# Optimization experiments

Measured on AMD Instinct MI355X. Metric: run time of the kernel, lower is better.

## Reference

```python
import jax, jax.numpy as jnp
import numpy as np

TEMPERATURE = 0.07
NUM_HARD_NEGATIVES = 5
BATCH, DIM = 4096, 768


def setup_inputs() -> dict:
    key = jax.random.key(0)
    k1, k2 = jax.random.split(key)
    return {
        "text_emb": jax.random.normal(k1, (BATCH, DIM), dtype=jnp.float32),
        "table_emb": jax.random.normal(k2, (BATCH, DIM), dtype=jnp.float32),
    }


def _ttcl_loss(text_emb, table_emb):
    # F.normalize(dim=1)
    t = text_emb / jnp.linalg.norm(text_emb, axis=1, keepdims=True)
    z = table_emb / jnp.linalg.norm(table_emb, axis=1, keepdims=True)
    sim = z @ t.T  # [B, B], sim[i, j] = <table_i, text_j>
    B = sim.shape[0]
    pos = jnp.diagonal(sim) / TEMPERATURE  # [B], <text_i, table_i> == <table_i, text_i>
    diag_mask = jnp.eye(B, dtype=bool)
    neg_inf = jnp.finfo(sim.dtype).min

    def hard_neg_loss(neg_rows):
        # neg_rows[i] holds the B candidate negatives for sample i; exclude self.
        neg = jnp.where(diag_mask, neg_inf, neg_rows)
        top_vals, _ = jax.lax.top_k(neg, NUM_HARD_NEGATIVES)  # [B, k]
        logits = jnp.concatenate([pos[:, None], top_vals / TEMPERATURE], axis=1)  # [B, k+1]
        # cross_entropy with label 0 == -log_softmax(logits)[:, 0]
        return -jax.nn.log_softmax(logits, axis=1)[:, 0]

    # t2z: negatives for i are sim[j][i], j != i  -> column i -> rows of sim.T
    loss_t2z = jnp.sum(hard_neg_loss(sim.T))
    # z2t: negatives for i are sim[i][j], j != i  -> row i
    loss_z2t = jnp.sum(hard_neg_loss(sim))
    loss = (loss_t2z + loss_z2t) / (2 * B)
    return loss, sim


def reference(text_emb, table_emb):
    return _ttcl_loss(text_emb, table_emb)
```

## Files before the change

kernel.cpp:

```cpp
#include <hip/hip_runtime.h>
#include <stdint.h>
#include <math.h>

#define BSZ 4096
#define DIM 768
#define TEMP 0.07f

typedef short short8 __attribute__((ext_vector_type(8)));
typedef short short4v __attribute__((ext_vector_type(4)));
typedef float f32x4 __attribute__((ext_vector_type(4)));


__device__ __forceinline__ uint16_t f2bf(float f) {
  uint32_t u = __float_as_uint(f);
  uint32_t r = (u + 0x7FFFu + ((u >> 16) & 1u)) >> 16;
  return (uint16_t)r;
}

__device__ __forceinline__ void gll16(const void* g, void* l) {
  __builtin_amdgcn_global_load_lds(
      (__attribute__((address_space(1))) void*)(uintptr_t)g,
      (__attribute__((address_space(3))) void*)l,
      16, 0, 0);
}

__device__ __forceinline__ void ins5(float v, float& a, float& b, float& c,
                                     float& d, float& e) {
  if (v > e) {
    e = v;
    if (e > d) { float t = d; d = e; e = t;
      if (d > c) { t = c; c = d; d = t;
        if (c > b) { t = b; b = c; c = t;
          if (b > a) { t = a; a = b; b = t; } } } }
  }
}

__device__ __forceinline__ void sins5(float v, float& a, float& b, float& c,
                                      float& d, float& e) {
  float t;
  t = fmaxf(a, v); v = fminf(a, v); a = t;
  t = fmaxf(b, v); v = fminf(b, v); b = t;
  t = fmaxf(c, v); v = fminf(c, v); c = t;
  t = fmaxf(d, v); v = fminf(d, v); d = t;
  e = fmaxf(e, v);
}

__global__ __launch_bounds__(192) void k_norm(const float* __restrict__ text,
                                              const float* __restrict__ table,
                                              uint16_t* __restrict__ tn,
                                              uint16_t* __restrict__ zn) {
  int row = blockIdx.x & (BSZ - 1);
  bool isTable = blockIdx.x >= BSZ;
  const float* src = (isTable ? table : text) + (size_t)row * DIM;
  uint16_t* dst = (isTable ? zn : tn) + (size_t)row * DIM;
  int tid = threadIdx.x;

  f32x4 v = *(const f32x4*)(src + tid * 4);
  float ss = v[0] * v[0] + v[1] * v[1] + v[2] * v[2] + v[3] * v[3];
  #pragma unroll
  for (int off = 32; off >= 1; off >>= 1) ss += __shfl_xor(ss, off);
  __shared__ float wss[3];
  if ((tid & 63) == 0) wss[tid >> 6] = ss;
  __syncthreads();
  float inv = rsqrtf(wss[0] + wss[1] + wss[2]);
  short4v o;
  o[0] = (short)f2bf(v[0] * inv);
  o[1] = (short)f2bf(v[1] * inv);
  o[2] = (short)f2bf(v[2] * inv);
  o[3] = (short)f2bf(v[3] * inv);
  *(short4v*)(dst + tid * 4) = o;
}

__global__ __launch_bounds__(512, 2) void k_gemm(const uint16_t* __restrict__ Zb,
                                                 const uint16_t* __restrict__ Tb,
                                                 float* __restrict__ sim) {
  extern __shared__ __attribute__((aligned(16))) char lds[];

  int tid = threadIdx.x;
  int wave = tid >> 6, lane = tid & 63;
  int wm = wave >> 2, wn = wave & 3;

  int bid = blockIdx.x;
  int xcd = bid & 7, li = bid >> 3;
  int brow = (((xcd >> 1) << 2) + (li >> 3)) << 8;
  int bcol = (((xcd & 1) << 3) + (li & 7)) << 8;

  f32x4 acc[8][4] = {};

  const uint16_t* gA = Zb + (size_t)brow * DIM;
  const uint16_t* gB = Tb + (size_t)bcol * DIM;

  int r7 = lane & 7;
  int kqg = lane >> 4;
  int rlo = lane & 15;

  int srow = (wave << 5) + (lane >> 3);
  int sc = ((lane & 7) ^ (srow & 7)) << 3;

  auto SA = [&](int t, int bb, int j) {
    gll16(gA + (size_t)(srow + j * 8) * DIM + t * 64 + sc,
          lds + bb + (wave << 12) + (j << 10));
  };
  auto SB = [&](int t, int bb, int j) {
    gll16(gB + (size_t)(srow + j * 8) * DIM + t * 64 + sc,
          lds + bb + 32768 + (wave << 12) + (j << 10));
  };

  auto LOADB = [&](int bb, short8 (&bf)[2][4]) {
    const char* Bb = lds + bb + 32768;
    #pragma unroll
    for (int ks = 0; ks < 2; ++ks) {
      int ch = (((ks << 2) + kqg) ^ r7) << 4;
      #pragma unroll
      for (int n = 0; n < 4; ++n) {
        int R = (wn << 6) + (n << 4) + rlo;
        bf[ks][n] = *(const short8*)(Bb + (R << 7) + ch);
      }
    }
  };
  auto PHASE = [&](int bb, int mlo, short8 (&bf)[2][4]) {
    __builtin_amdgcn_s_setprio(1);
    #pragma unroll
    for (int ks = 0; ks < 2; ++ks) {
      int ch = (((ks << 2) + kqg) ^ r7) << 4;
      #pragma unroll
      for (int mm = 0; mm < 4; ++mm) {
        int R = (wm << 7) + ((mlo + mm) << 4) + rlo;
        short8 af = *(const short8*)(lds + bb + (R << 7) + ch);
        #pragma unroll
        for (int n = 0; n < 4; ++n)
          acc[mlo + mm][n] = __builtin_amdgcn_mfma_f32_16x16x32_bf16(
              af, bf[ks][n], acc[mlo + mm][n], 0, 0, 0);
      }
    }
    __builtin_amdgcn_s_setprio(0);
  };

  #pragma unroll
  for (int j = 0; j < 4; ++j) { SA(0, 0, j); SB(0, 0, j); }
  #pragma unroll
  for (int j = 0; j < 4; ++j) { SA(1, 65536, j); SB(1, 65536, j); }
  asm volatile("s_waitcnt vmcnt(8)" ::: "memory");
  __builtin_amdgcn_s_barrier();

  #pragma unroll 2
  for (int t = 0; t < 10; ++t) {
    int bb = (t & 1) << 16;
    short8 bf[2][4];
    LOADB(bb, bf);
    PHASE(bb, 0, bf);
    __builtin_amdgcn_s_barrier();
    if ((wave & 2) == 0) {
      SA(t + 2, bb, 0); SA(t + 2, bb, 1); SA(t + 2, bb, 2); SA(t + 2, bb, 3);
    }
    SB(t + 2, bb, 0); SB(t + 2, bb, 1);
    SB(t + 2, bb, 2); SB(t + 2, bb, 3);
    PHASE(bb, 4, bf);
    __builtin_amdgcn_s_barrier();
    if ((wave & 2) != 0) {
      SA(t + 2, bb, 0); SA(t + 2, bb, 1); SA(t + 2, bb, 2); SA(t + 2, bb, 3);
    }
    asm volatile("s_waitcnt vmcnt(8)" ::: "memory");
    __builtin_amdgcn_s_barrier();
  }

  {
    short8 bf[2][4];
    LOADB(0, bf);
    PHASE(0, 0, bf);
    PHASE(0, 4, bf);
  }
  asm volatile("s_waitcnt vmcnt(0)" ::: "memory");
  __builtin_amdgcn_s_barrier();
  {
    short8 bf[2][4];
    LOADB(65536, bf);
    PHASE(65536, 0, bf);
    PHASE(65536, 4, bf);
  }

  int crow0 = brow + (wm << 7) + ((lane >> 4) << 2);
  int ccol0 = bcol + (wn << 6) + (lane & 15);
  #pragma unroll
  for (int m = 0; m < 8; ++m)
    #pragma unroll
    for (int n = 0; n < 4; ++n)
      #pragma unroll
      for (int r = 0; r < 4; ++r)
        sim[(size_t)(crow0 + m * 16 + r) * BSZ + (ccol0 + n * 16)] = acc[m][n][r];
}

__global__ __launch_bounds__(256) void k_tile(const float* __restrict__ sim,
                                              float* __restrict__ rp,
                                              float* __restrict__ cp) {
  extern __shared__ float l32[];
  int tid = threadIdx.x;

  int xcd = blockIdx.x & 7, li = blockIdx.x >> 3;
  int tr = ((xcd >> 1) << 4) + (li >> 4);
  int tc = ((xcd & 1) << 4) + (li & 15);
  int row0 = tr << 6, col0 = tc << 7;
  bool diag = ((tr >> 1) == tc);
  int lcbase = (tr & 1) << 6;

  int q = tid & 31;
  int g = tid >> 5;
  const float* gsrc = sim + (size_t)(row0 + (g << 3)) * BSZ + col0 + (q << 2);

  f32x4 v[8];
  #pragma unroll
  for (int k = 0; k < 8; ++k)
    v[k] = *(const f32x4*)(gsrc + (size_t)k * BSZ);

  #pragma unroll
  for (int k = 0; k < 8; ++k) {
    int r = (g << 3) + k;
    int lc = lcbase + r;
    if (diag && (lc >> 2) == q) v[k][lc & 3] = -1e30f;
    *(f32x4*)(l32 + (r << 7) + ((q ^ (r & 7)) << 2)) = v[k];
  }
  __syncthreads();

  {
    int row = tid >> 2, h = tid & 3;
    int rx = row & 7;
    const float* rb = l32 + (row << 7);
    float a0 = -1e30f, a1 = -1e30f, a2 = -1e30f, a3 = -1e30f, a4 = -1e30f;
    #pragma unroll
    for (int j = 0; j < 8; ++j) {
      int c16 = (h << 3) + j;
      f32x4 x = *(const f32x4*)(rb + ((c16 ^ rx) << 2));
      sins5(x[0], a0, a1, a2, a3, a4);
      sins5(x[1], a0, a1, a2, a3, a4);
      sins5(x[2], a0, a1, a2, a3, a4);
      sins5(x[3], a0, a1, a2, a3, a4);
    }
    #pragma unroll
    for (int xr = 1; xr <= 2; xr <<= 1) {
      float b0 = __shfl_xor(a0, xr), b1 = __shfl_xor(a1, xr),
            b2 = __shfl_xor(a2, xr), b3 = __shfl_xor(a3, xr),
            b4 = __shfl_xor(a4, xr);
      sins5(b0, a0, a1, a2, a3, a4);
      sins5(b1, a0, a1, a2, a3, a4);
      sins5(b2, a0, a1, a2, a3, a4);
      sins5(b3, a0, a1, a2, a3, a4);
      sins5(b4, a0, a1, a2, a3, a4);
    }
    if (h == 0) {
      float* pr = rp + ((size_t)(row0 + row) * 32 + tc) * 5;
      pr[0] = a0; pr[1] = a1; pr[2] = a2; pr[3] = a3; pr[4] = a4;
    }
  }

  {
    int c = tid >> 1, hf = tid & 1;
    int cc = c >> 2, cw = c & 3;
    float a0 = -1e30f, a1 = -1e30f, a2 = -1e30f, a3 = -1e30f, a4 = -1e30f;
    #pragma unroll 8
    for (int k = 0; k < 32; ++k) {
      int r = (hf << 5) + k;
      float x = l32[(r << 7) + (((cc ^ (r & 7)) << 2) | cw)];
      sins5(x, a0, a1, a2, a3, a4);
    }
    float b0 = __shfl_xor(a0, 1), b1 = __shfl_xor(a1, 1),
          b2 = __shfl_xor(a2, 1), b3 = __shfl_xor(a3, 1),
          b4 = __shfl_xor(a4, 1);
    sins5(b0, a0, a1, a2, a3, a4);
    sins5(b1, a0, a1, a2, a3, a4);
    sins5(b2, a0, a1, a2, a3, a4);
    sins5(b3, a0, a1, a2, a3, a4);
    sins5(b4, a0, a1, a2, a3, a4);
    if (hf == 0) {
      float* pc = cp + ((size_t)(col0 + c) * 64 + tr) * 5;
      pc[0] = a0; pc[1] = a1; pc[2] = a2; pc[3] = a3; pc[4] = a4;
    }
  }
}

__global__ __launch_bounds__(256) void k_merge(const float* __restrict__ sim,
                                               const float* __restrict__ rp,
                                               const float* __restrict__ cp,
                                               float* __restrict__ lossbuf) {
  int wave = threadIdx.x >> 6, lane = threadIdx.x & 63;
  int wid = blockIdx.x * 4 + wave;
  bool isCol = wid >= BSZ;
  int line = isCol ? wid - BSZ : wid;

  float t0 = -1e30f, t1 = -1e30f, t2 = -1e30f, t3 = -1e30f, t4 = -1e30f;
  if (isCol) {
    const float* src = cp + (size_t)line * 320;
    ins5(src[lane], t0, t1, t2, t3, t4);
    ins5(src[lane + 64], t0, t1, t2, t3, t4);
    ins5(src[lane + 128], t0, t1, t2, t3, t4);
    ins5(src[lane + 192], t0, t1, t2, t3, t4);
    ins5(src[lane + 256], t0, t1, t2, t3, t4);
  } else {
    const float* src = rp + (size_t)line * 160;
    ins5(src[lane], t0, t1, t2, t3, t4);
    ins5(src[lane + 64], t0, t1, t2, t3, t4);
    if (lane < 32) ins5(src[lane + 128], t0, t1, t2, t3, t4);
  }

  float top[5];
  #pragma unroll
  for (int e = 0; e < 5; e++) {
    float m = t0;
    #pragma unroll
    for (int off = 32; off >= 1; off >>= 1) m = fmaxf(m, __shfl_xor(m, off));
    unsigned long long msk = __ballot(t0 == m);
    int owner = __ffsll(msk) - 1;
    if (lane == owner) { t0 = t1; t1 = t2; t2 = t3; t3 = t4; t4 = -1e30f; }
    top[e] = m;
  }

  if (lane == 0) {
    float pos = sim[(size_t)line * BSZ + line] / TEMP;
    float l0 = top[0] / TEMP, l1 = top[1] / TEMP, l2 = top[2] / TEMP,
          l3 = top[3] / TEMP, l4 = top[4] / TEMP;
    float mx = fmaxf(pos, fmaxf(fmaxf(l0, l1), fmaxf(fmaxf(l2, l3), l4)));
    float s = expf(pos - mx) + expf(l0 - mx) + expf(l1 - mx) +
              expf(l2 - mx) + expf(l3 - mx) + expf(l4 - mx);
    lossbuf[wid] = mx + logf(s) - pos;
  }
}

__global__ __launch_bounds__(256) void k_reduce(const float* __restrict__ losses,
                                                float* __restrict__ out) {
  int tid = threadIdx.x;
  float s = 0.f;
  for (int i = tid; i < 2 * BSZ; i += 256) s += losses[i];
  #pragma unroll
  for (int off = 32; off >= 1; off >>= 1) s += __shfl_xor(s, off);
  __shared__ float wss[4];
  if ((tid & 63) == 0) wss[tid >> 6] = s;
  __syncthreads();
  if (tid == 0) out[0] = (wss[0] + wss[1] + wss[2] + wss[3]) / (2.0f * BSZ);
}

extern "C" void kernel_launch(void* const* d_in, const int* in_sizes, int n_in,
                              void* d_out, int out_size, void* d_ws, size_t ws_size,
                              hipStream_t stream) {
  const float* text = (const float*)d_in[0];
  const float* table = (const float*)d_in[1];
  float* out = (float*)d_out;
  float* sim = out + 1;

  uint16_t* Zb = (uint16_t*)d_ws;
  uint16_t* Tb = Zb + (size_t)BSZ * DIM;
  float* lossbuf = (float*)(Tb + (size_t)BSZ * DIM);

  float* rp = (float*)d_ws;
  float* cp = rp + (size_t)BSZ * 32 * 5;

  k_norm<<<2 * BSZ, 192, 0, stream>>>(text, table, Tb, Zb);
  k_gemm<<<(BSZ / 256) * (BSZ / 256), 512, 131072, stream>>>(Zb, Tb, sim);
  k_tile<<<(BSZ / 64) * (BSZ / 128), 256, 32768, stream>>>(sim, rp, cp);
  k_merge<<<2 * BSZ / 4, 256, 0, stream>>>(sim, rp, cp, lossbuf);
  k_reduce<<<1, 256, 0, stream>>>(lossbuf, out);
}
```

Measured before the change: 82.88 us.

## Single-buffer GEMM LDS staging to halve shared memory and raise occupancy

The bf16 GEMM drops its double-buffered 128KB LDS staging for a single 64KB buffer. Refills of the next K tile are split across extra barriers so B and the two halves of A are reloaded as each is consumed. The launch-bounds occupancy hint rises from 2 to 4 so more blocks can share a CU. The cost is less overlap between global loads and MFMA work, more barriers per iteration, and possible register pressure or spills from the tighter bound. The grid is only 256 blocks, so the extra occupancy may never be used.

Result: slower. 289.6 us (+249.5%).

```diff
diff --git a/kernel.cpp b/kernel.cpp
--- a/kernel.cpp
+++ b/kernel.cpp
@@ -71,7 +71,7 @@
   *(short4v*)(dst + tid * 4) = o;
 }
 
-__global__ __launch_bounds__(512, 2) void k_gemm(const uint16_t* __restrict__ Zb,
+__global__ __launch_bounds__(512, 4) void k_gemm(const uint16_t* __restrict__ Zb,
                                                  const uint16_t* __restrict__ Tb,
                                                  float* __restrict__ sim) {
   extern __shared__ __attribute__((aligned(16))) char lds[];
@@ -96,18 +96,19 @@
 
   int srow = (wave << 5) + (lane >> 3);
   int sc = ((lane & 7) ^ (srow & 7)) << 3;
-
-  auto SA = [&](int t, int bb, int j) {
+  bool ownH1 = (wave & 2) == 0;
+
+  auto SA = [&](int t, int j) {
     gll16(gA + (size_t)(srow + j * 8) * DIM + t * 64 + sc,
-          lds + bb + (wave << 12) + (j << 10));
+          lds + (wave << 12) + (j << 10));
   };
-  auto SB = [&](int t, int bb, int j) {
+  auto SB = [&](int t, int j) {
     gll16(gB + (size_t)(srow + j * 8) * DIM + t * 64 + sc,
-          lds + bb + 32768 + (wave << 12) + (j << 10));
+          lds + 32768 + (wave << 12) + (j << 10));
   };
 
-  auto LOADB = [&](int bb, short8 (&bf)[2][4]) {
-    const char* Bb = lds + bb + 32768;
+  auto LOADB = [&](short8 (&bf)[2][4]) {
+    const char* Bb = lds + 32768;
     #pragma unroll
     for (int ks = 0; ks < 2; ++ks) {
       int ch = (((ks << 2) + kqg) ^ r7) << 4;
@@ -118,7 +119,7 @@
       }
     }
   };
-  auto PHASE = [&](int bb, int mlo, short8 (&bf)[2][4]) {
+  auto PHASE = [&](int mlo, short8 (&bf)[2][4]) {
     __builtin_amdgcn_s_setprio(1);
     #pragma unroll
     for (int ks = 0; ks < 2; ++ks) {
@@ -126,7 +127,7 @@
       #pragma unroll
       for (int mm = 0; mm < 4; ++mm) {
         int R = (wm << 7) + ((mlo + mm) << 4) + rlo;
-        short8 af = *(const short8*)(lds + bb + (R << 7) + ch);
+        short8 af = *(const short8*)(lds + (R << 7) + ch);
         #pragma unroll
         for (int n = 0; n < 4; ++n)
           acc[mlo + mm][n] = __builtin_amdgcn_mfma_f32_16x16x32_bf16(
@@ -136,48 +137,43 @@
     __builtin_amdgcn_s_setprio(0);
   };
 
-  #pragma unroll
-  for (int j = 0; j < 4; ++j) { SA(0, 0, j); SB(0, 0, j); }
-  #pragma unroll
-  for (int j = 0; j < 4; ++j) { SA(1, 65536, j); SB(1, 65536, j); }
-  asm volatile("s_waitcnt vmcnt(8)" ::: "memory");
-  __builtin_amdgcn_s_barrier();
-
-  #pragma unroll 2
-  for (int t = 0; t < 10; ++t) {
-    int bb = (t & 1) << 16;
+#define BAR __builtin_amdgcn_s_barrier()
+#define VM4 asm volatile("s_waitcnt vmcnt(4)" ::: "memory")
+
+  #pragma unroll
+  for (int j = 0; j < 4; ++j) { SA(0, j); SB(0, j); }
+  asm volatile("s_waitcnt vmcnt(0)" ::: "memory");
+  BAR;
+
+  #pragma unroll 1
+  for (int t = 0; t <= 10; ++t) {
     short8 bf[2][4];
-    LOADB(bb, bf);
-    PHASE(bb, 0, bf);
-    __builtin_amdgcn_s_barrier();
-    if ((wave & 2) == 0) {
-      SA(t + 2, bb, 0); SA(t + 2, bb, 1); SA(t + 2, bb, 2); SA(t + 2, bb, 3);
-    }
-    SB(t + 2, bb, 0); SB(t + 2, bb, 1);
-    SB(t + 2, bb, 2); SB(t + 2, bb, 3);
-    PHASE(bb, 4, bf);
-    __builtin_amdgcn_s_barrier();
-    if ((wave & 2) != 0) {
-      SA(t + 2, bb, 0); SA(t + 2, bb, 1); SA(t + 2, bb, 2); SA(t + 2, bb, 3);
-    }
-    asm volatile("s_waitcnt vmcnt(8)" ::: "memory");
-    __builtin_amdgcn_s_barrier();
+    LOADB(bf);
+    BAR;
+    SB(t + 1, 0); SB(t + 1, 1); SB(t + 1, 2); SB(t + 1, 3);
+    if (ownH1) VM4;
+    BAR;
+    PHASE(0, bf);
+    BAR;
+    if (ownH1) { SA(t + 1, 0); SA(t + 1, 1); SA(t + 1, 2); SA(t + 1, 3); }
+    else VM4;
+    BAR;
+    PHASE(4, bf);
+    BAR;
+    if (!ownH1) { SA(t + 1, 0); SA(t + 1, 1); SA(t + 1, 2); SA(t + 1, 3); }
+    if (t < 10) VM4;
+    else asm volatile("s_waitcnt vmcnt(0)" ::: "memory");
+    BAR;
   }
 
   {
     short8 bf[2][4];
-    LOADB(0, bf);
-    PHASE(0, 0, bf);
-    PHASE(0, 4, bf);
-  }
-  asm volatile("s_waitcnt vmcnt(0)" ::: "memory");
-  __builtin_amdgcn_s_barrier();
-  {
-    short8 bf[2][4];
-    LOADB(65536, bf);
-    PHASE(65536, 0, bf);
-    PHASE(65536, 4, bf);
-  }
+    LOADB(bf);
+    PHASE(0, bf);
+    PHASE(4, bf);
+  }
+#undef BAR
+#undef VM4
 
   int crow0 = brow + (wm << 7) + ((lane >> 4) << 2);
   int ccol0 = bcol + (wn << 6) + (lane & 15);
@@ -353,7 +349,7 @@
   float* cp = rp + (size_t)BSZ * 32 * 5;
 
   k_norm<<<2 * BSZ, 192, 0, stream>>>(text, table, Tb, Zb);
-  k_gemm<<<(BSZ / 256) * (BSZ / 256), 512, 131072, stream>>>(Zb, Tb, sim);
+  k_gemm<<<(BSZ / 256) * (BSZ / 256), 512, 65536, stream>>>(Zb, Tb, sim);
   k_tile<<<(BSZ / 64) * (BSZ / 128), 256, 32768, stream>>>(sim, rp, cp);
   k_merge<<<2 * BSZ / 4, 256, 0, stream>>>(sim, rp, cp, lossbuf);
   k_reduce<<<1, 256, 0, stream>>>(lossbuf, out);
```

## Fuse final loss reduction into merge via atomics and simplify GEMM prefetch schedule

Applied to the files above, without the earlier changes.

The separate single-block reduce kernel is removed. Each merge block now sums its four per-line losses in shared memory and atomically adds the scaled total to the output scalar, which the norm kernel zeroes first. Separately, the GEMM main loop no longer interleaves the next-tile global-to-LDS prefetches between its two MFMA phases. All waves now issue every prefetch after one barrier, which also drops a barrier per iteration. This saves a kernel launch but adds float-atomic contention and nondeterministic summation order, and the prefetch may now overlap less with compute.

New measurement: 93.65 us. 1.13x slower.

```diff
diff --git a/kernel.cpp b/kernel.cpp
--- a/kernel.cpp
+++ b/kernel.cpp
@@ -48,7 +48,9 @@
 __global__ __launch_bounds__(192) void k_norm(const float* __restrict__ text,
                                               const float* __restrict__ table,
                                               uint16_t* __restrict__ tn,
-                                              uint16_t* __restrict__ zn) {
+                                              uint16_t* __restrict__ zn,
+                                              float* __restrict__ out) {
+  if (blockIdx.x == 0 && threadIdx.x == 0) out[0] = 0.f;
   int row = blockIdx.x & (BSZ - 1);
   bool isTable = blockIdx.x >= BSZ;
   const float* src = (isTable ? table : text) + (size_t)row * DIM;
@@ -149,17 +151,10 @@
     short8 bf[2][4];
     LOADB(bb, bf);
     PHASE(bb, 0, bf);
-    __builtin_amdgcn_s_barrier();
-    if ((wave & 2) == 0) {
-      SA(t + 2, bb, 0); SA(t + 2, bb, 1); SA(t + 2, bb, 2); SA(t + 2, bb, 3);
-    }
-    SB(t + 2, bb, 0); SB(t + 2, bb, 1);
-    SB(t + 2, bb, 2); SB(t + 2, bb, 3);
     PHASE(bb, 4, bf);
     __builtin_amdgcn_s_barrier();
-    if ((wave & 2) != 0) {
-      SA(t + 2, bb, 0); SA(t + 2, bb, 1); SA(t + 2, bb, 2); SA(t + 2, bb, 3);
-    }
+    SA(t + 2, bb, 0); SA(t + 2, bb, 1); SA(t + 2, bb, 2); SA(t + 2, bb, 3);
+    SB(t + 2, bb, 0); SB(t + 2, bb, 1); SB(t + 2, bb, 2); SB(t + 2, bb, 3);
     asm volatile("s_waitcnt vmcnt(8)" ::: "memory");
     __builtin_amdgcn_s_barrier();
   }
@@ -280,7 +275,7 @@
 __global__ __launch_bounds__(256) void k_merge(const float* __restrict__ sim,
                                                const float* __restrict__ rp,
                                                const float* __restrict__ cp,
-                                               float* __restrict__ lossbuf) {
+                                               float* __restrict__ out) {
   int wave = threadIdx.x >> 6, lane = threadIdx.x & 63;
   int wid = blockIdx.x * 4 + wave;
   bool isCol = wid >= BSZ;
@@ -313,6 +308,7 @@
     top[e] = m;
   }
 
+  __shared__ float ls[4];
   if (lane == 0) {
     float pos = sim[(size_t)line * BSZ + line] / TEMP;
     float l0 = top[0] / TEMP, l1 = top[1] / TEMP, l2 = top[2] / TEMP,
@@ -320,21 +316,11 @@
     float mx = fmaxf(pos, fmaxf(fmaxf(l0, l1), fmaxf(fmaxf(l2, l3), l4)));
     float s = expf(pos - mx) + expf(l0 - mx) + expf(l1 - mx) +
               expf(l2 - mx) + expf(l3 - mx) + expf(l4 - mx);
-    lossbuf[wid] = mx + logf(s) - pos;
-  }
-}
-
-__global__ __launch_bounds__(256) void k_reduce(const float* __restrict__ losses,
-                                                float* __restrict__ out) {
-  int tid = threadIdx.x;
-  float s = 0.f;
-  for (int i = tid; i < 2 * BSZ; i += 256) s += losses[i];
-  #pragma unroll
-  for (int off = 32; off >= 1; off >>= 1) s += __shfl_xor(s, off);
-  __shared__ float wss[4];
-  if ((tid & 63) == 0) wss[tid >> 6] = s;
+    ls[wave] = mx + logf(s) - pos;
+  }
   __syncthreads();
-  if (tid == 0) out[0] = (wss[0] + wss[1] + wss[2] + wss[3]) / (2.0f * BSZ);
+  if (threadIdx.x == 0)
+    atomicAdd(out, (ls[0] + ls[1] + ls[2] + ls[3]) * (0.5f / BSZ));
 }
 
 extern "C" void kernel_launch(void* const* d_in, const int* in_sizes, int n_in,
@@ -347,14 +333,12 @@
 
   uint16_t* Zb = (uint16_t*)d_ws;
   uint16_t* Tb = Zb + (size_t)BSZ * DIM;
-  float* lossbuf = (float*)(Tb + (size_t)BSZ * DIM);
 
   float* rp = (float*)d_ws;
   float* cp = rp + (size_t)BSZ * 32 * 5;
 
-  k_norm<<<2 * BSZ, 192, 0, stream>>>(text, table, Tb, Zb);
+  k_norm<<<2 * BSZ, 192, 0, stream>>>(text, table, Tb, Zb, out);
   k_gemm<<<(BSZ / 256) * (BSZ / 256), 512, 131072, stream>>>(Zb, Tb, sim);
   k_tile<<<(BSZ / 64) * (BSZ / 128), 256, 32768, stream>>>(sim, rp, cp);
-  k_merge<<<2 * BSZ / 4, 256, 0, stream>>>(sim, rp, cp, lossbuf);
-  k_reduce<<<1, 256, 0, stream>>>(lossbuf, out);
-}
+  k_merge<<<2 * BSZ / 4, 256, 0, stream>>>(sim, rp, cp, out);
+}
```
